# Kernel tuning notes

Measured on AMD Instinct MI355X. Metric: run time of the kernel, lower is better.

## Reference

```python
import jax, jax.numpy as jnp
import numpy as np

B, N, C_IN, C_OUT, T, K = 16, 128, 64, 128, 256, 9
PAD = (K - 1) // 2


def conv1d(x, w, b, pad):
    # x: (n, c_in, t), w: (c_out, c_in, k) -> (n, c_out, t)
    y = jax.lax.conv_general_dilated(x, w, (1,), [(pad, pad)],
                                     dimension_numbers=('NCH', 'OIH', 'NCH'))
    return y + b[None, :, None]


def setup_inputs() -> dict:
    key = jax.random.key(0)
    ks = jax.random.split(key, 10)
    xav = lambda k, shape, fan_in, fan_out: jax.random.uniform(
        k, shape, jnp.float32, -1.0, 1.0) * np.sqrt(6.0 / (fan_in + fan_out))
    return {
        'x': jax.random.normal(ks[0], (B, N, C_IN, T), jnp.float32),
        'adjacency': jax.random.uniform(ks[1], (B, N, N), jnp.float32),
        'w_t1': xav(ks[2], (C_OUT, C_IN, K), C_IN * K, C_OUT * K),
        'b_t1': jnp.zeros((C_OUT,), jnp.float32),
        'w_sp': xav(ks[3], (C_OUT, C_OUT), C_OUT, C_OUT),
        'b_sp': jnp.zeros((C_OUT,), jnp.float32),
        'w_t2': xav(ks[4], (C_OUT, C_OUT, K), C_OUT * K, C_OUT * K),
        'b_t2': jnp.zeros((C_OUT,), jnp.float32),
        'w_res': xav(ks[5], (C_OUT, C_IN, 1), C_IN, C_OUT),
        'b_res': jnp.zeros((C_OUT,), jnp.float32),
    }


def reference(x, adjacency, w_t1, b_t1, w_sp, b_sp, w_t2, b_t2, w_res, b_res):
    b, n, c_in, t = x.shape
    xr = x.reshape(b * n, c_in, t)
    # temporal1 + relu
    h = jax.nn.relu(conv1d(xr, w_t1, b_t1, PAD))            # (b*n, c_out, t)
    c_out = h.shape[1]
    h = h.reshape(b, n, c_out, t).transpose(0, 3, 1, 2)      # (b, t, n, c)
    # spatial graph conv, batched over all timesteps at once
    support = jnp.einsum('btnc,co->btno', h, w_sp)
    h = jnp.einsum('bnm,btmo->btno', adjacency, support) + b_sp
    h = jax.nn.relu(h)
    h = h.transpose(0, 2, 3, 1).reshape(b * n, c_out, t)     # (b*n, c, t)
    # temporal2
    h = conv1d(h, w_t2, b_t2, PAD)
    # residual 1x1 conv (in_channels != out_channels)
    res = conv1d(xr, w_res, b_res, 0)
    out = (h + res).reshape(b, n, c_out, t)
    # dropout: identity in eval mode
    return out
```

## Files before the change

kernel.cpp:

```cpp
#include <hip/hip_runtime.h>

#define B_ 16
#define N_ 128
#define CI_ 64
#define CO_ 128
#define T_ 256
#define K_ 9

typedef __attribute__((ext_vector_type(8))) __bf16 bf16x8;
typedef __attribute__((ext_vector_type(4))) float f32x4;
typedef __attribute__((ext_vector_type(8))) unsigned short ushort8;

__device__ __forceinline__ unsigned short tobf(float f) {
  return __builtin_bit_cast(unsigned short, (__bf16)f);
}
__device__ __forceinline__ int swzs(int row, int col0) {
  return ((col0 >> 3) ^ (row & 7)) << 3;
}
__device__ __forceinline__ int swz(int row, int col) {
  return (((col >> 3) ^ (row & 7)) << 3) | (col & 7);
}
#define FRAG(p, idx) (*(const bf16x8*)((p) + (size_t)(idx) * 8))

__global__ __launch_bounds__(256) void k_prep(
    const float* __restrict__ w1, const float* __restrict__ w2,
    const float* __restrict__ wsp, const float* __restrict__ wr,
    const float* __restrict__ adj,
    unsigned short* __restrict__ w1f, unsigned short* __restrict__ w2f,
    unsigned short* __restrict__ wrf, unsigned short* __restrict__ wspf,
    unsigned short* __restrict__ adjf) {
  int idx = blockIdx.x * 256 + threadIdx.x;
  int stride = gridDim.x * 256;
  for (int i = idx; i < 73728; i += stride) {
    int e = i & 7, lane = (i >> 3) & 63, ni = (i >> 9) & 3, cg = (i >> 11) & 1;
    int kb = (i >> 12) & 1, k = i >> 13;
    int co = cg * 64 + ni * 16 + (lane & 15), ci = kb * 32 + (lane >> 4) * 8 + e;
    w1f[i] = tobf(w1[(co * 64 + ci) * 9 + k]);
  }
  for (int i = idx; i < 147456; i += stride) {
    int e = i & 7, lane = (i >> 3) & 63, ni = (i >> 9) & 3, cg = (i >> 11) & 1;
    int kb = (i >> 12) & 3, k = i >> 14;
    int co = cg * 64 + ni * 16 + (lane & 15), c = kb * 32 + (lane >> 4) * 8 + e;
    w2f[i] = tobf(w2[(co * 128 + c) * 9 + k]);
  }
  for (int i = idx; i < 8192; i += stride) {
    int e = i & 7, lane = (i >> 3) & 63, ni = (i >> 9) & 3, cg = (i >> 11) & 1;
    int kb = i >> 12;
    int co = cg * 64 + ni * 16 + (lane & 15), ci = kb * 32 + (lane >> 4) * 8 + e;
    wrf[i] = tobf(wr[co * 64 + ci]);
  }
  for (int i = idx; i < 16384; i += stride) {
    int e = i & 7, lane = (i >> 3) & 63, mi = (i >> 9) & 3, og = (i >> 11) & 1;
    int kb = i >> 12;
    int o = og * 64 + mi * 16 + (lane & 15), c = kb * 32 + (lane >> 4) * 8 + e;
    wspf[i] = tobf(wsp[c * 128 + o]);
  }
  for (int i = idx; i < 262144; i += stride) {
    int e = i & 7, lane = (i >> 3) & 63, ni = (i >> 9) & 1, ng = (i >> 10) & 3;
    int kb = (i >> 12) & 3, b = i >> 14;
    int nn = ng * 32 + ni * 16 + (lane & 15), m = kb * 32 + (lane >> 4) * 8 + e;
    adjf[i] = tobf(adj[(b * 128 + nn) * 128 + m]);
  }
}

__global__ __launch_bounds__(256) void k_xT(const float* __restrict__ x,
                                            unsigned short* __restrict__ xT) {
  __shared__ unsigned short tr[T_ * 66];
  int tid = threadIdx.x, bn = blockIdx.x;
  const float* xb = x + (size_t)bn * CI_ * T_;
  for (int i = tid; i < CI_ * T_; i += 256) {
    int ci = i >> 8, t = i & 255;
    tr[t * 66 + ci] = tobf(xb[i]);
  }
  __syncthreads();
  unsigned short* o = xT + (size_t)bn * T_ * CI_;
  for (int i = tid; i < T_ * CI_; i += 256) {
    int t = i >> 6, p = i & 63;
    o[i] = tr[t * 66 + p];
  }
}

__global__ __launch_bounds__(256, 3) void k_conv1(
    const unsigned short* __restrict__ xT, const unsigned short* __restrict__ w1f,
    const float* __restrict__ b1, unsigned short* __restrict__ h1) {
  __shared__ alignas(16) char smem[17408];
  unsigned short* xs = (unsigned short*)smem;
  unsigned short* ot = (unsigned short*)smem;

  int tid = threadIdx.x, blk = blockIdx.x;
  int bn = blk >> 1, th = blk & 1, t0 = th * 128;
  ushort8 zv = {0, 0, 0, 0, 0, 0, 0, 0};
  const unsigned short* xg = xT + (size_t)bn * T_ * CI_;
  for (int i = tid; i < 136 * 8; i += 256) {
    int r = i >> 3, s = i & 7;
    int t = t0 - 4 + r;
    ushort8 v = (t >= 0 && t < T_) ? *(const ushort8*)&xg[t * 64 + s * 8] : zv;
    *(ushort8*)&xs[r * 64 + ((s ^ (r & 7)) << 3)] = v;
  }
  int lane = tid & 63, wid = tid >> 6;
  int lrow = lane & 15, lk8 = (lane >> 4) * 8, lq = lane >> 4;
  int trow0 = (wid >> 1) * 64, cg = wid & 1;
  const unsigned short* wp = w1f + (size_t)(cg * 256 + lane) * 8;

  f32x4 acc[4][4];
#pragma unroll
  for (int ni = 0; ni < 4; ++ni) {
    float bv = b1[cg * 64 + ni * 16 + lrow];
    f32x4 ini = {bv, bv, bv, bv};
#pragma unroll
    for (int mi = 0; mi < 4; ++mi) acc[mi][ni] = ini;
  }
  __syncthreads();

#pragma unroll 2
  for (int it = 0; it < 18; ++it) {
    int k = it >> 1;
    int col0 = (it & 1) * 32 + lk8;
    bf16x8 bfr[4];
#pragma unroll
    for (int ni = 0; ni < 4; ++ni) bfr[ni] = FRAG(wp, it * 512 + ni * 64);
    bf16x8 a[4];
#pragma unroll
    for (int mi = 0; mi < 4; ++mi) {
      int r = trow0 + mi * 16 + lrow + k;
      a[mi] = *(const bf16x8*)&xs[r * 64 + swzs(r, col0)];
    }
#pragma unroll
    for (int mi = 0; mi < 4; ++mi)
#pragma unroll
      for (int ni = 0; ni < 4; ++ni)
        acc[mi][ni] = __builtin_amdgcn_mfma_f32_16x16x32_bf16(
            a[mi], bfr[ni], acc[mi][ni], 0, 0, 0);
  }
  __syncthreads();

  int b = bn >> 7, n = bn & 127;
  for (int ch = 0; ch < 2; ++ch) {
    if ((trow0 >> 6) == ch) {
#pragma unroll
      for (int mi = 0; mi < 4; ++mi)
#pragma unroll
        for (int ni = 0; ni < 4; ++ni) {
          int col = cg * 64 + ni * 16 + lrow;
#pragma unroll
          for (int r = 0; r < 4; ++r) {
            int row = mi * 16 + lq * 4 + r;
            float v = acc[mi][ni][r];
            v = v > 0.f ? v : 0.f;
            ot[row * 128 + swz(row, col)] = tobf(v);
          }
        }
    }
    __syncthreads();
    for (int i = tid; i < 64 * 16; i += 256) {
      int tl = i >> 4, s = i & 15;
      int t = t0 + ch * 64 + tl;
      int ls = s ^ (tl & 7);
      size_t gb = ((size_t)((b * T_ + t) * N_ + n)) << 7;
      *(ushort8*)&h1[gb + ls * 8] = *(const ushort8*)&ot[tl * 128 + s * 8];
    }
    __syncthreads();
  }
}

__global__ __launch_bounds__(512) void k_spatial(
    unsigned short* __restrict__ h1, const unsigned short* __restrict__ adjf,
    const unsigned short* __restrict__ wspf, const float* __restrict__ bsp) {
  __shared__ alignas(16) char smem[65536];
  unsigned short* h1t = (unsigned short*)smem;
  unsigned short* stt = h1t + 16384;
  unsigned short* ot = h1t;

  int tid = threadIdx.x, blk = blockIdx.x;
  int b = blk >> 8;
  unsigned short* h1g = h1 + ((size_t)blk << 14);
  const ushort8* hsrc = (const ushort8*)h1g;
  for (int i = tid; i < 2048; i += 512) {
    int n = i >> 4, s = i & 15;
    *(ushort8*)&h1t[n * 128 + ((s ^ (n & 7)) << 3)] = hsrc[i];
  }
  int lane = tid & 63, wid = tid >> 6;
  int lrow = lane & 15, lk8 = (lane >> 4) * 8, lq = lane >> 4;
  int og = wid >> 2, ng = wid & 3;
  const unsigned short* sp = wspf + (size_t)(og * 256 + lane) * 8;
  const unsigned short* ap = adjf + ((size_t)b * 2048 + ng * 128 + lane) * 8;

  float bspv[4];
#pragma unroll
  for (int oi = 0; oi < 4; ++oi) bspv[oi] = bsp[og * 64 + oi * 16 + lrow];
  __syncthreads();

  f32x4 acc1[4][2];
#pragma unroll
  for (int mi = 0; mi < 4; ++mi)
#pragma unroll
    for (int ni = 0; ni < 2; ++ni) acc1[mi][ni] = (f32x4){0.f, 0.f, 0.f, 0.f};
#pragma unroll
  for (int kb = 0; kb < 4; ++kb) {
    int col0 = kb * 32 + lk8;
    bf16x8 aw[4];
#pragma unroll
    for (int mi = 0; mi < 4; ++mi) aw[mi] = FRAG(sp, kb * 512 + mi * 64);
#pragma unroll
    for (int ni = 0; ni < 2; ++ni) {
      int rn = ng * 32 + ni * 16 + lrow;
      bf16x8 bh = *(const bf16x8*)&h1t[rn * 128 + swzs(rn, col0)];
#pragma unroll
      for (int mi = 0; mi < 4; ++mi)
        acc1[mi][ni] = __builtin_amdgcn_mfma_f32_16x16x32_bf16(
            aw[mi], bh, acc1[mi][ni], 0, 0, 0);
    }
  }
#pragma unroll
  for (int mi = 0; mi < 4; ++mi)
#pragma unroll
    for (int ni = 0; ni < 2; ++ni) {
      int ncol = ng * 32 + ni * 16 + lrow;
#pragma unroll
      for (int r = 0; r < 4; ++r) {
        int o = og * 64 + mi * 16 + lq * 4 + r;
        stt[o * 128 + swz(o, ncol)] = tobf(acc1[mi][ni][r]);
      }
    }
  __syncthreads();

  f32x4 acc2[2][4];
#pragma unroll
  for (int oi = 0; oi < 4; ++oi) {
    f32x4 ini = {bspv[oi], bspv[oi], bspv[oi], bspv[oi]};
#pragma unroll
    for (int ni = 0; ni < 2; ++ni) acc2[ni][oi] = ini;
  }
#pragma unroll
  for (int kb = 0; kb < 4; ++kb) {
    int col0 = kb * 32 + lk8;
    bf16x8 aa[2];
#pragma unroll
    for (int ni = 0; ni < 2; ++ni) aa[ni] = FRAG(ap, kb * 512 + ni * 64);
#pragma unroll
    for (int oi = 0; oi < 4; ++oi) {
      int ro = og * 64 + oi * 16 + lrow;
      bf16x8 bs = *(const bf16x8*)&stt[ro * 128 + swzs(ro, col0)];
#pragma unroll
      for (int ni = 0; ni < 2; ++ni)
        acc2[ni][oi] = __builtin_amdgcn_mfma_f32_16x16x32_bf16(
            aa[ni], bs, acc2[ni][oi], 0, 0, 0);
    }
  }
  __syncthreads();
#pragma unroll
  for (int ni = 0; ni < 2; ++ni)
#pragma unroll
    for (int oi = 0; oi < 4; ++oi) {
      int o = og * 64 + oi * 16 + lrow;
#pragma unroll
      for (int r = 0; r < 4; ++r) {
        int nrow = ng * 32 + ni * 16 + lq * 4 + r;
        float v = acc2[ni][oi][r];
        v = v > 0.f ? v : 0.f;
        ot[nrow * 128 + swz(nrow, o)] = tobf(v);
      }
    }
  __syncthreads();
  for (int i = tid; i < 2048; i += 512) {
    int n = i >> 4, s = i & 15;
    int ls = s ^ (n & 7);
    *(ushort8*)&h1g[n * 128 + ls * 8] = *(const ushort8*)&ot[n * 128 + s * 8];
  }
}

__global__ __launch_bounds__(256, 3) void k_conv2(
    const unsigned short* __restrict__ H2, const unsigned short* __restrict__ xT,
    const unsigned short* __restrict__ w2f, const unsigned short* __restrict__ wrf,
    const float* __restrict__ b2, const float* __restrict__ br,
    float* __restrict__ out) {
  __shared__ alignas(16) char smem[34816];
  unsigned short* h2t = (unsigned short*)smem;
  float* ot = (float*)smem;

  int tid = threadIdx.x, blk = blockIdx.x;
  int bn = blk >> 1, th = blk & 1, t0 = th * 128;
  int b = bn >> 7, n = bn & 127;
  ushort8 zv = {0, 0, 0, 0, 0, 0, 0, 0};
  for (int i = tid; i < 136 * 16; i += 256) {
    int tl = i >> 4, s = i & 15;
    int t = t0 - 4 + tl;
    ushort8 v = zv;
    if (t >= 0 && t < T_)
      v = *(const ushort8*)&H2[(((size_t)((b * T_ + t) * N_ + n)) << 7) + s * 8];
    *(ushort8*)&h2t[tl * 128 + ((s ^ (tl & 7)) << 3)] = v;
  }
  int lane = tid & 63, wid = tid >> 6;
  int lrow = lane & 15, lk8 = (lane >> 4) * 8, lq = lane >> 4;
  int trow0 = (wid >> 1) * 64, cg = wid & 1;
  const unsigned short* wp = w2f + (size_t)(cg * 256 + lane) * 8;
  const unsigned short* rp = wrf + (size_t)(cg * 256 + lane) * 8;

  f32x4 acc[4][4];
#pragma unroll
  for (int ni = 0; ni < 4; ++ni) {
    float bv = b2[cg * 64 + ni * 16 + lrow] + br[cg * 64 + ni * 16 + lrow];
    f32x4 ini = {bv, bv, bv, bv};
#pragma unroll
    for (int mi = 0; mi < 4; ++mi) acc[mi][ni] = ini;
  }
  __syncthreads();

#pragma unroll 4
  for (int it = 0; it < 36; ++it) {
    int k = it >> 2;
    int col0 = (it & 3) * 32 + lk8;
    bf16x8 bfr[4];
#pragma unroll
    for (int ni = 0; ni < 4; ++ni) bfr[ni] = FRAG(wp, it * 512 + ni * 64);
    bf16x8 a[4];
#pragma unroll
    for (int mi = 0; mi < 4; ++mi) {
      int r = trow0 + mi * 16 + lrow + k;
      a[mi] = *(const bf16x8*)&h2t[r * 128 + swzs(r, col0)];
    }
#pragma unroll
    for (int mi = 0; mi < 4; ++mi)
#pragma unroll
      for (int ni = 0; ni < 4; ++ni)
        acc[mi][ni] = __builtin_amdgcn_mfma_f32_16x16x32_bf16(
            a[mi], bfr[ni], acc[mi][ni], 0, 0, 0);
  }

  const unsigned short* xg = xT + ((size_t)bn * T_ + t0) * 64;
#pragma unroll
  for (int kb = 0; kb < 2; ++kb) {
    int c0 = kb * 32 + lk8;
    bf16x8 bfr[4];
#pragma unroll
    for (int ni = 0; ni < 4; ++ni) bfr[ni] = FRAG(rp, kb * 512 + ni * 64);
    bf16x8 a[4];
#pragma unroll
    for (int mi = 0; mi < 4; ++mi)
      a[mi] = *(const bf16x8*)&xg[(trow0 + mi * 16 + lrow) * 64 + c0];
#pragma unroll
    for (int mi = 0; mi < 4; ++mi)
#pragma unroll
      for (int ni = 0; ni < 4; ++ni)
        acc[mi][ni] = __builtin_amdgcn_mfma_f32_16x16x32_bf16(
            a[mi], bfr[ni], acc[mi][ni], 0, 0, 0);
  }
  __syncthreads();

  for (int ch = 0; ch < 2; ++ch) {
    if (cg == ch) {
#pragma unroll
      for (int mi = 0; mi < 4; ++mi)
#pragma unroll
        for (int ni = 0; ni < 4; ++ni) {
          int col = ni * 16 + lrow;
          int tl = trow0 + mi * 16 + lq * 4;
          *(f32x4*)&ot[col * 128 + ((((tl >> 2) ^ (col & 7))) << 2)] = acc[mi][ni];
        }
    }
    __syncthreads();
    for (int i = tid; i < 64 * 32; i += 256) {
      int col = i >> 5, s = i & 31;
      float4 v = *(const float4*)&ot[col * 128 + s * 4];
      int lslot = s ^ (col & 7);
      *(float4*)&out[((size_t)bn * 128 + ch * 64 + col) * 256 + t0 + lslot * 4] = v;
    }
    __syncthreads();
  }
}

extern "C" void kernel_launch(void* const* d_in, const int* in_sizes, int n_in,
                              void* d_out, int out_size, void* d_ws, size_t ws_size,
                              hipStream_t stream) {
  const float* x = (const float*)d_in[0];
  const float* adj = (const float*)d_in[1];
  const float* w_t1 = (const float*)d_in[2];
  const float* b_t1 = (const float*)d_in[3];
  const float* w_sp = (const float*)d_in[4];
  const float* b_sp = (const float*)d_in[5];
  const float* w_t2 = (const float*)d_in[6];
  const float* b_t2 = (const float*)d_in[7];
  const float* w_res = (const float*)d_in[8];
  const float* b_res = (const float*)d_in[9];
  float* out = (float*)d_out;

  unsigned short* wsu = (unsigned short*)d_ws;
  unsigned short* h1 = wsu;
  unsigned short* xT = h1 + 67108864;
  unsigned short* w1f = xT + 33554432;
  unsigned short* w2f = w1f + 73728;
  unsigned short* wrf = w2f + 147456;
  unsigned short* wspf = wrf + 8192;
  unsigned short* adjf = wspf + 16384;

  k_prep<<<512, 256, 0, stream>>>(w_t1, w_t2, w_sp, w_res, adj,
                                  w1f, w2f, wrf, wspf, adjf);
  k_xT<<<B_ * N_, 256, 0, stream>>>(x, xT);
  k_conv1<<<B_ * N_ * 2, 256, 0, stream>>>(xT, w1f, b_t1, h1);
  k_spatial<<<B_ * T_, 512, 0, stream>>>(h1, adjf, wspf, b_sp);
  k_conv2<<<B_ * N_ * 2, 256, 0, stream>>>(h1, xT, w2f, wrf, b_t2, b_res, out);
}
```

Baseline: 373.3 us.

## Fuse x transpose into conv1, use direct-to-LDS loads, pipeline conv2 weights

Removes the separate k_xT kernel. conv1 now reads fp32 x directly, converts and transposes it into LDS, then writes the bf16 xT copy that conv2's residual needs. k_spatial and k_conv2 stage tiles with global_load_lds (direct global-to-LDS), pre-swizzling the source address, and conv2 zero-fills its out-of-range halo rows explicitly. conv2's main loop is hand-unrolled by two with double-buffered weight fragments, and occupancy hints rise to 4 blocks per SIMD, which risks register pressure and spills.

Result: faster. 360.3 us (-3.5%).

```diff
diff --git a/kernel.cpp b/kernel.cpp
--- a/kernel.cpp
+++ b/kernel.cpp
@@ -21,6 +21,12 @@
   return (((col >> 3) ^ (row & 7)) << 3) | (col & 7);
 }
 #define FRAG(p, idx) (*(const bf16x8*)((p) + (size_t)(idx) * 8))
+
+__device__ __forceinline__ void gload16(const void* g, void* l) {
+  __builtin_amdgcn_global_load_lds(
+      (const __attribute__((address_space(1))) void*)g,
+      (__attribute__((address_space(3))) void*)l, 16, 0, 0);
+}
 
 __global__ __launch_bounds__(256) void k_prep(
     const float* __restrict__ w1, const float* __restrict__ w2,
@@ -63,40 +69,36 @@
   }
 }
 
-__global__ __launch_bounds__(256) void k_xT(const float* __restrict__ x,
-                                            unsigned short* __restrict__ xT) {
-  __shared__ unsigned short tr[T_ * 66];
-  int tid = threadIdx.x, bn = blockIdx.x;
-  const float* xb = x + (size_t)bn * CI_ * T_;
-  for (int i = tid; i < CI_ * T_; i += 256) {
-    int ci = i >> 8, t = i & 255;
-    tr[t * 66 + ci] = tobf(xb[i]);
-  }
-  __syncthreads();
-  unsigned short* o = xT + (size_t)bn * T_ * CI_;
-  for (int i = tid; i < T_ * CI_; i += 256) {
-    int t = i >> 6, p = i & 63;
-    o[i] = tr[t * 66 + p];
-  }
-}
-
-__global__ __launch_bounds__(256, 3) void k_conv1(
-    const unsigned short* __restrict__ xT, const unsigned short* __restrict__ w1f,
-    const float* __restrict__ b1, unsigned short* __restrict__ h1) {
+__global__ __launch_bounds__(256, 4) void k_conv1(
+    const float* __restrict__ x, const unsigned short* __restrict__ w1f,
+    const float* __restrict__ b1, unsigned short* __restrict__ h1,
+    unsigned short* __restrict__ xT) {
   __shared__ alignas(16) char smem[17408];
   unsigned short* xs = (unsigned short*)smem;
   unsigned short* ot = (unsigned short*)smem;
 
   int tid = threadIdx.x, blk = blockIdx.x;
   int bn = blk >> 1, th = blk & 1, t0 = th * 128;
-  ushort8 zv = {0, 0, 0, 0, 0, 0, 0, 0};
-  const unsigned short* xg = xT + (size_t)bn * T_ * CI_;
-  for (int i = tid; i < 136 * 8; i += 256) {
-    int r = i >> 3, s = i & 7;
+  const float* xb = x + (size_t)bn * CI_ * T_;
+#pragma unroll
+  for (int it = 0; it < 8; ++it) {
+    int idx = it * 256 + tid;
+    int ci = idx >> 5, ch = idx & 31;
+    float4 v = *(const float4*)&xb[ci * 256 + t0 + ch * 4];
+    int r = 4 + ch * 4;
+    xs[(r + 0) * 64 + swz(r + 0, ci)] = tobf(v.x);
+    xs[(r + 1) * 64 + swz(r + 1, ci)] = tobf(v.y);
+    xs[(r + 2) * 64 + swz(r + 2, ci)] = tobf(v.z);
+    xs[(r + 3) * 64 + swz(r + 3, ci)] = tobf(v.w);
+  }
+  for (int i = tid; i < 512; i += 256) {
+    int r8 = i >> 6, ci = i & 63;
+    int r = (r8 < 4) ? r8 : 128 + r8;
     int t = t0 - 4 + r;
-    ushort8 v = (t >= 0 && t < T_) ? *(const ushort8*)&xg[t * 64 + s * 8] : zv;
-    *(ushort8*)&xs[r * 64 + ((s ^ (r & 7)) << 3)] = v;
-  }
+    float v = (t >= 0 && t < T_) ? xb[ci * 256 + t] : 0.f;
+    xs[r * 64 + swz(r, ci)] = tobf(v);
+  }
+
   int lane = tid & 63, wid = tid >> 6;
   int lrow = lane & 15, lk8 = (lane >> 4) * 8, lq = lane >> 4;
   int trow0 = (wid >> 1) * 64, cg = wid & 1;
@@ -111,6 +113,16 @@
     for (int mi = 0; mi < 4; ++mi) acc[mi][ni] = ini;
   }
   __syncthreads();
+
+  {
+    unsigned short* xo = xT + ((size_t)bn * T_ + t0) * 64;
+    for (int i = tid; i < 1024; i += 256) {
+      int tl = i >> 3, s = i & 7;
+      int r = tl + 4;
+      *(ushort8*)&xo[tl * 64 + s * 8] =
+          *(const ushort8*)&xs[r * 64 + ((s ^ (r & 7)) << 3)];
+    }
+  }
 
 #pragma unroll 2
   for (int it = 0; it < 18; ++it) {
@@ -163,7 +175,7 @@
   }
 }
 
-__global__ __launch_bounds__(512) void k_spatial(
+__global__ __launch_bounds__(512, 4) void k_spatial(
     unsigned short* __restrict__ h1, const unsigned short* __restrict__ adjf,
     const unsigned short* __restrict__ wspf, const float* __restrict__ bsp) {
   __shared__ alignas(16) char smem[65536];
@@ -174,10 +186,11 @@
   int tid = threadIdx.x, blk = blockIdx.x;
   int b = blk >> 8;
   unsigned short* h1g = h1 + ((size_t)blk << 14);
-  const ushort8* hsrc = (const ushort8*)h1g;
-  for (int i = tid; i < 2048; i += 512) {
+#pragma unroll
+  for (int it = 0; it < 4; ++it) {
+    int i = it * 512 + tid;
     int n = i >> 4, s = i & 15;
-    *(ushort8*)&h1t[n * 128 + ((s ^ (n & 7)) << 3)] = hsrc[i];
+    gload16(h1g + n * 128 + ((s ^ (n & 7)) << 3), h1t + ((i & ~63) << 3));
   }
   int lane = tid & 63, wid = tid >> 6;
   int lrow = lane & 15, lk8 = (lane >> 4) * 8, lq = lane >> 4;
@@ -269,7 +282,7 @@
   }
 }
 
-__global__ __launch_bounds__(256, 3) void k_conv2(
+__global__ __launch_bounds__(256, 4) void k_conv2(
     const unsigned short* __restrict__ H2, const unsigned short* __restrict__ xT,
     const unsigned short* __restrict__ w2f, const unsigned short* __restrict__ wrf,
     const float* __restrict__ b2, const float* __restrict__ br,
@@ -282,18 +295,29 @@
   int bn = blk >> 1, th = blk & 1, t0 = th * 128;
   int b = bn >> 7, n = bn & 127;
   ushort8 zv = {0, 0, 0, 0, 0, 0, 0, 0};
-  for (int i = tid; i < 136 * 16; i += 256) {
-    int tl = i >> 4, s = i & 15;
-    int t = t0 - 4 + tl;
-    ushort8 v = zv;
-    if (t >= 0 && t < T_)
-      v = *(const ushort8*)&H2[(((size_t)((b * T_ + t) * N_ + n)) << 7) + s * 8];
-    *(ushort8*)&h2t[tl * 128 + ((s ^ (tl & 7)) << 3)] = v;
-  }
+  size_t h2base = ((size_t)(b * T_ + t0 - 4) * N_ + n) << 7;
+#pragma unroll
+  for (int it = 0; it < 9; ++it) {
+    int i = it * 256 + tid;
+    if (i < 2176) {
+      int tl = i >> 4, s = i & 15;
+      int t = t0 - 4 + tl;
+      if (t >= 0 && t < T_) {
+        gload16(H2 + h2base + (size_t)tl * (N_ * CO_) + ((s ^ (tl & 7)) << 3),
+                h2t + ((i & ~63) << 3));
+      }
+    }
+  }
+  if (tid < 64) {
+    int tl = (th == 0) ? (tid >> 4) : (132 + (tid >> 4));
+    int s = tid & 15;
+    *(ushort8*)&h2t[tl * 128 + s * 8] = zv;
+  }
+
   int lane = tid & 63, wid = tid >> 6;
   int lrow = lane & 15, lk8 = (lane >> 4) * 8, lq = lane >> 4;
   int trow0 = (wid >> 1) * 64, cg = wid & 1;
-  const unsigned short* wp = w2f + (size_t)(cg * 256 + lane) * 8;
+  const unsigned short* wpc = w2f + (size_t)(cg * 256 + lane) * 8;
   const unsigned short* rp = wrf + (size_t)(cg * 256 + lane) * 8;
 
   f32x4 acc[4][4];
@@ -304,27 +328,50 @@
 #pragma unroll
     for (int mi = 0; mi < 4; ++mi) acc[mi][ni] = ini;
   }
-  __syncthreads();
-
-#pragma unroll 4
-  for (int it = 0; it < 36; ++it) {
-    int k = it >> 2;
-    int col0 = (it & 3) * 32 + lk8;
-    bf16x8 bfr[4];
-#pragma unroll
-    for (int ni = 0; ni < 4; ++ni) bfr[ni] = FRAG(wp, it * 512 + ni * 64);
-    bf16x8 a[4];
-#pragma unroll
-    for (int mi = 0; mi < 4; ++mi) {
-      int r = trow0 + mi * 16 + lrow + k;
-      a[mi] = *(const bf16x8*)&h2t[r * 128 + swzs(r, col0)];
-    }
-#pragma unroll
-    for (int mi = 0; mi < 4; ++mi)
-#pragma unroll
-      for (int ni = 0; ni < 4; ++ni)
-        acc[mi][ni] = __builtin_amdgcn_mfma_f32_16x16x32_bf16(
-            a[mi], bfr[ni], acc[mi][ni], 0, 0, 0);
+  bf16x8 bA[4], bB[4];
+#pragma unroll
+  for (int ni = 0; ni < 4; ++ni) bA[ni] = FRAG(wpc, ni * 64);
+  __syncthreads();
+
+  for (int it = 0; it < 36; it += 2) {
+#pragma unroll
+    for (int ni = 0; ni < 4; ++ni) bB[ni] = FRAG(wpc, 512 + ni * 64);
+    {
+      int k = it >> 2, col0 = (it & 3) * 32 + lk8;
+      bf16x8 a[4];
+#pragma unroll
+      for (int mi = 0; mi < 4; ++mi) {
+        int r = trow0 + mi * 16 + lrow + k;
+        a[mi] = *(const bf16x8*)&h2t[r * 128 + swzs(r, col0)];
+      }
+#pragma unroll
+      for (int mi = 0; mi < 4; ++mi)
+#pragma unroll
+        for (int ni = 0; ni < 4; ++ni)
+          acc[mi][ni] = __builtin_amdgcn_mfma_f32_16x16x32_bf16(
+              a[mi], bA[ni], acc[mi][ni], 0, 0, 0);
+    }
+    if (it + 2 < 36) {
+#pragma unroll
+      for (int ni = 0; ni < 4; ++ni) bA[ni] = FRAG(wpc, 1024 + ni * 64);
+    }
+    {
+      int it1 = it + 1;
+      int k = it1 >> 2, col0 = (it1 & 3) * 32 + lk8;
+      bf16x8 a[4];
+#pragma unroll
+      for (int mi = 0; mi < 4; ++mi) {
+        int r = trow0 + mi * 16 + lrow + k;
+        a[mi] = *(const bf16x8*)&h2t[r * 128 + swzs(r, col0)];
+      }
+#pragma unroll
+      for (int mi = 0; mi < 4; ++mi)
+#pragma unroll
+        for (int ni = 0; ni < 4; ++ni)
+          acc[mi][ni] = __builtin_amdgcn_mfma_f32_16x16x32_bf16(
+              a[mi], bB[ni], acc[mi][ni], 0, 0, 0);
+    }
+    wpc += 8192;
   }
 
   const unsigned short* xg = xT + ((size_t)bn * T_ + t0) * 64;
@@ -395,8 +442,7 @@
 
   k_prep<<<512, 256, 0, stream>>>(w_t1, w_t2, w_sp, w_res, adj,
                                   w1f, w2f, wrf, wspf, adjf);
-  k_xT<<<B_ * N_, 256, 0, stream>>>(x, xT);
-  k_conv1<<<B_ * N_ * 2, 256, 0, stream>>>(xT, w1f, b_t1, h1);
+  k_conv1<<<B_ * N_ * 2, 256, 0, stream>>>(x, w1f, b_t1, h1, xT);
   k_spatial<<<B_ * T_, 512, 0, stream>>>(h1, adjf, wspf, b_sp);
   k_conv2<<<B_ * N_ * 2, 256, 0, stream>>>(h1, xT, w2f, wrf, b_t2, b_res, out);
 }
```
